# Optimization experiments

Hardware: AMD Instinct MI355X
Metric: run time of the kernel (lower is better)

## Reference

```python
import jax, jax.numpy as jnp
import numpy as np

# Dimensions (match init_kwargs)
B, N, D = 128, 256, 256   # batch, n_agents, obs_dim
MSG = 64                  # msg_dim
CD = 32                   # compressed_dim = int(msg_dim * 0.5)
K = 8                     # top-k recipients
H1, H2 = 128, 256         # msg_gen hidden, receiver hidden


def setup_inputs() -> dict:
    key = jax.random.key(0)
    ks = jax.random.split(key, 16)
    s = 0.02
    # All weights stored (in_features, out_features): y = x @ W + b
    return {
        "obs_all": jax.random.normal(ks[0], (B, N, D), dtype=jnp.float32),
        "W1": jax.random.normal(ks[1], (D, H1), dtype=jnp.float32) * s,
        "b1": jnp.zeros((H1,), jnp.float32),
        "W2": jax.random.normal(ks[2], (H1, MSG), dtype=jnp.float32) * s,
        "b2": jnp.zeros((MSG,), jnp.float32),
        "Wc": jax.random.normal(ks[3], (MSG, CD), dtype=jnp.float32) * s,
        "bc": jnp.zeros((CD,), jnp.float32),
        "Wd": jax.random.normal(ks[4], (CD, MSG), dtype=jnp.float32) * s,
        "bd": jnp.zeros((MSG,), jnp.float32),
        "Wbil": jax.random.normal(ks[5], (D, D), dtype=jnp.float32) * s,  # Bilinear weight (out=1)
        "bbil": jnp.zeros((), jnp.float32),
        "Wr1": jax.random.normal(ks[6], (D + MSG, H2), dtype=jnp.float32) * s,
        "br1": jnp.zeros((H2,), jnp.float32),
        "Wr2": jax.random.normal(ks[7], (H2, D), dtype=jnp.float32) * s,
        "br2": jnp.zeros((D,), jnp.float32),
    }


def reference(obs_all, W1, b1, W2, b2, Wc, bc, Wd, bd, Wbil, bbil, Wr1, br1, Wr2, br2):
    # send: msg_gen MLP -> compress -> decompress (all agents at once)
    h = jax.nn.relu(jnp.einsum('bnd,dh->bnh', obs_all, W1) + b1)
    full_msg = jnp.einsum('bnh,hm->bnm', h, W2) + b2          # (B, N, MSG)
    compressed = jnp.einsum('bnm,mc->bnc', full_msg, Wc) + bc  # (B, N, CD)
    msgs = jnp.einsum('bnc,cm->bnm', compressed, Wd) + bd      # (B, N, MSG)

    # pairwise bilinear relevance: scores[b,i,j] = obs_i^T Wbil obs_j + bias
    tmp = jnp.einsum('bid,de->bie', obs_all, Wbil)
    scores = jnp.einsum('bie,bje->bij', tmp, obs_all) + bbil   # (B, N, N)

    # top-k gating: softmax over the k selected scores, zeros elsewhere
    topk_vals, topk_idx = jax.lax.top_k(scores, K)             # (B, N, K)
    gate_vals = jax.nn.softmax(topk_vals, axis=-1)             # (B, N, K)

    # weighted aggregation of selected messages (honor top-k sparsity:
    # gather the K messages per receiver instead of building dense gates)
    sel_msgs = jax.vmap(lambda m, ix: m[ix])(msgs, topk_idx)   # (B, N, K, MSG)
    agg = jnp.einsum('bik,bikm->bim', gate_vals, sel_msgs)     # (B, N, MSG)

    # receive: MLP over [obs, aggregated message]
    combined = jnp.concatenate([obs_all, agg], axis=-1)        # (B, N, D+MSG)
    r = jax.nn.relu(jnp.einsum('bnc,ch->bnh', combined, Wr1) + br1)
    enriched = jnp.einsum('bnh,hd->bnd', r, Wr2) + br2          # (B, N, D)
    return enriched
```

## Files before the change

kernel.cpp:

```cpp
#include <hip/hip_runtime.h>
#include <cstddef>

#define BB   128
#define NN   256
#define DIMD 256
#define MSG  64
#define CDIM 32
#define TOPK 8
#define H1D  128
#define H2D  256
#define BN   (BB*NN)

typedef unsigned short u16;
typedef u16   u16x4  __attribute__((ext_vector_type(4)));
typedef u16   u16x8  __attribute__((ext_vector_type(8)));
typedef short short8 __attribute__((ext_vector_type(8)));
typedef float f32x4  __attribute__((ext_vector_type(4)));

__device__ __forceinline__ u16 f2bf(float f) {
    return (u16)((__float_as_uint(f) + 0x8000u) >> 16);
}
__device__ __forceinline__ float bf2f(u16 u) {
    return __uint_as_float(((unsigned)u) << 16);
}
__device__ __forceinline__ u16 bf2key(u16 b) {
    return (u16)(b ^ ((b & 0x8000u) ? 0xFFFFu : 0x8000u));
}
__device__ __forceinline__ u16 key2bf(u16 k) {
    return (u16)(k ^ ((k & 0x8000u) ? 0x8000u : 0xFFFFu));
}
#define MFMA16(a,b,c) __builtin_amdgcn_mfma_f32_16x16x32_bf16((a),(b),(c),0,0,0)


__global__ __launch_bounds__(256) void prep_w_k(
    const float* __restrict__ W1, const float* __restrict__ W2,
    const float* __restrict__ Wc, const float* __restrict__ Wd,
    const float* __restrict__ Wb, const float* __restrict__ Wr1,
    const float* __restrict__ Wr2,
    u16* __restrict__ Wp1, u16* __restrict__ Wp2, u16* __restrict__ Wpc,
    u16* __restrict__ Wpd, u16* __restrict__ WpB, u16* __restrict__ Wpr1,
    u16* __restrict__ Wpr2)
{
    const int t = blockIdx.x * 256 + threadIdx.x;
    const float* src; u16* dst; int I, os, loc;
    if      (t <  32768) { src = W1;  dst = Wp1;  I = 256; os = 7; loc = t; }
    else if (t <  40960) { src = W2;  dst = Wp2;  I = 128; os = 6; loc = t - 32768; }
    else if (t <  43008) { src = Wc;  dst = Wpc;  I = 64;  os = 5; loc = t - 40960; }
    else if (t <  45056) { src = Wd;  dst = Wpd;  I = 32;  os = 6; loc = t - 43008; }
    else if (t < 110592) { src = Wb;  dst = WpB;  I = 256; os = 8; loc = t - 45056; }
    else if (t < 192512) { src = Wr1; dst = Wpr1; I = 320; os = 8; loc = t - 110592; }
    else                 { src = Wr2; dst = Wpr2; I = 256; os = 8; loc = t - 192512; }
    const int i = loc >> os;
    const int o = loc & ((1 << os) - 1);
    const int nt = o >> 4, ls = o & 15;
    const int KB = I >> 5;
    const int kk = i >> 5, q = (i & 31) >> 3, j = i & 7;
    dst[((size_t)(nt*KB + kk)*64 + q*16 + ls)*8 + j] = f2bf(src[loc]);
}

__global__ __launch_bounds__(256) __attribute__((amdgpu_waves_per_eu(4, 4)))
void sendpack_k(
    const float* __restrict__ obs, u16* __restrict__ obs_p,
    const u16* __restrict__ Wp1, const float* __restrict__ b1,
    const u16* __restrict__ Wp2, const float* __restrict__ b2,
    const u16* __restrict__ Wpc, const float* __restrict__ bc,
    const u16* __restrict__ Wpd, const float* __restrict__ bd,
    u16* __restrict__ msgs_bf)
{
    __shared__ __align__(16) u16 sO[32][264];
    __shared__ __align__(16) u16 sH[32][136];
    __shared__ __align__(16) u16 sF[32][72];
    __shared__ __align__(16) u16 sC[32][40];
    const int t = threadIdx.x;
    const int w = t >> 6, l = t & 63, q = l >> 4, ls = l & 15;
    const int row0 = blockIdx.x * 32;
    const int tile0 = blockIdx.x * 2;

    {
        const float4* src = (const float4*)(obs + (size_t)row0 * 256);
        #pragma unroll
        for (int i = 0; i < 8; ++i) {
            const int idx = t + 256*i;
            const int r = idx >> 6, c4 = idx & 63;
            const float4 v = src[idx];
            u16x4 o;
            o[0] = f2bf(v.x); o[1] = f2bf(v.y); o[2] = f2bf(v.z); o[3] = f2bf(v.w);
            *(u16x4*)&sO[r][c4*4] = o;
        }
    }
    __syncthreads();
    {
        #pragma unroll
        for (int i = 0; i < 4; ++i) {
            const int u = t + 256*i;
            const int tile = u >> 9, kk = (u >> 6) & 7, lane = u & 63;
            const u16x8 v = *(const u16x8*)&sO[tile*16 + (lane & 15)][kk*32 + (lane >> 4)*8];
            *(u16x8*)(obs_p + (size_t)(tile0 + tile)*4096 + (size_t)(kk*64 + lane)*8) = v;
        }
    }
    {
        f32x4 acc[2][2];
        #pragma unroll
        for (int mi = 0; mi < 2; ++mi)
            #pragma unroll
            for (int nn = 0; nn < 2; ++nn) acc[mi][nn] = (f32x4){0,0,0,0};
        short8 cb[2];
        #pragma unroll
        for (int nn = 0; nn < 2; ++nn)
            cb[nn] = *(const short8*)(Wp1 + ((size_t)((w*2+nn)*8))*512 + l*8);
        #pragma unroll
        for (int kk = 0; kk < 8; ++kk) {
            short8 nb[2];
            if (kk < 7) {
                #pragma unroll
                for (int nn = 0; nn < 2; ++nn)
                    nb[nn] = *(const short8*)(Wp1 + ((size_t)((w*2+nn)*8 + kk+1))*512 + l*8);
            }
            short8 a[2];
            a[0] = *(const short8*)&sO[ls][kk*32 + q*8];
            a[1] = *(const short8*)&sO[16 + ls][kk*32 + q*8];
            #pragma unroll
            for (int mi = 0; mi < 2; ++mi)
                #pragma unroll
                for (int nn = 0; nn < 2; ++nn)
                    acc[mi][nn] = MFMA16(a[mi], cb[nn], acc[mi][nn]);
            if (kk < 7) {
                #pragma unroll
                for (int nn = 0; nn < 2; ++nn) cb[nn] = nb[nn];
            }
        }
        #pragma unroll
        for (int nn = 0; nn < 2; ++nn) {
            const float bv = b1[(w*2+nn)*16 + ls];
            #pragma unroll
            for (int mi = 0; mi < 2; ++mi)
                #pragma unroll
                for (int r = 0; r < 4; ++r)
                    sH[mi*16 + q*4 + r][(w*2+nn)*16 + ls] = f2bf(fmaxf(acc[mi][nn][r] + bv, 0.0f));
        }
    }
    __syncthreads();
    {
        f32x4 acc[2];
        acc[0] = (f32x4){0,0,0,0}; acc[1] = (f32x4){0,0,0,0};
        #pragma unroll
        for (int kk = 0; kk < 4; ++kk) {
            const int k0 = kk * 32;
            short8 a[2];
            a[0] = *(const short8*)(&sH[ls][k0 + q*8]);
            a[1] = *(const short8*)(&sH[16 + ls][k0 + q*8]);
            const short8 bf = *(const short8*)(Wp2 + ((size_t)(w*4 + kk)*64 + l)*8);
            acc[0] = MFMA16(a[0], bf, acc[0]);
            acc[1] = MFMA16(a[1], bf, acc[1]);
        }
        const float bv = b2[w*16 + ls];
        #pragma unroll
        for (int mi = 0; mi < 2; ++mi)
            #pragma unroll
            for (int r = 0; r < 4; ++r)
                sF[mi*16 + q*4 + r][w*16 + ls] = f2bf(acc[mi][r] + bv);
    }
    __syncthreads();
    if (w < 2) {
        f32x4 acc[2];
        acc[0] = (f32x4){0,0,0,0}; acc[1] = (f32x4){0,0,0,0};
        #pragma unroll
        for (int kk = 0; kk < 2; ++kk) {
            const int k0 = kk * 32;
            short8 a[2];
            a[0] = *(const short8*)(&sF[ls][k0 + q*8]);
            a[1] = *(const short8*)(&sF[16 + ls][k0 + q*8]);
            const short8 bf = *(const short8*)(Wpc + ((size_t)(w*2 + kk)*64 + l)*8);
            acc[0] = MFMA16(a[0], bf, acc[0]);
            acc[1] = MFMA16(a[1], bf, acc[1]);
        }
        const float bv = bc[w*16 + ls];
        #pragma unroll
        for (int mi = 0; mi < 2; ++mi)
            #pragma unroll
            for (int r = 0; r < 4; ++r)
                sC[mi*16 + q*4 + r][w*16 + ls] = f2bf(acc[mi][r] + bv);
    }
    __syncthreads();
    {
        f32x4 acc[2];
        acc[0] = (f32x4){0,0,0,0}; acc[1] = (f32x4){0,0,0,0};
        short8 a[2];
        a[0] = *(const short8*)(&sC[ls][q*8]);
        a[1] = *(const short8*)(&sC[16 + ls][q*8]);
        const short8 bf = *(const short8*)(Wpd + ((size_t)w*64 + l)*8);
        acc[0] = MFMA16(a[0], bf, acc[0]);
        acc[1] = MFMA16(a[1], bf, acc[1]);
        const float bv = bd[w*16 + ls];
        #pragma unroll
        for (int mi = 0; mi < 2; ++mi)
            #pragma unroll
            for (int r = 0; r < 4; ++r)
                msgs_bf[(size_t)(row0 + mi*16 + q*4 + r)*MSG + w*16 + ls] = f2bf(acc[mi][r] + bv);
    }
}

__global__ __launch_bounds__(512) __attribute__((amdgpu_waves_per_eu(4, 4)))
void relrecv_k(
    const u16* __restrict__ obs_p, const u16* __restrict__ WpB,
    const float* __restrict__ bbil, const u16* __restrict__ msgs_bf,
    const u16* __restrict__ Wpr1, const float* __restrict__ br1,
    const u16* __restrict__ Wpr2, const float* __restrict__ br2,
    float* __restrict__ out)
{
    __shared__ __align__(16) u16 sS[64][264];
    __shared__ __align__(16) u16 sA[64][72];
    __shared__ __align__(16) u16 sObs[16384];
    __shared__ float sG[64][8];
    __shared__ unsigned short sI[64][8];
    const int t = threadIdx.x;
    const int w = t >> 6, l = t & 63, q = l >> 4, ls = l & 15;
    const int bid = blockIdx.x;
    const int xcd = bid & 7, idx = bid >> 3;
    const int b   = xcd * 16 + (idx >> 2);
    const int mc  = idx & 3;
    const int row0g = b * NN + mc * 64;
    const int mt0   = b * 16 + mc * 4;

    short8 pb[4][2];

    {
        const u16x8* src = (const u16x8*)(obs_p + (size_t)mt0 * 4096);
        #pragma unroll
        for (int i = 0; i < 4; ++i)
            *(u16x8*)&sObs[(t + 512*i) * 8] = src[t + 512*i];
    }
    #pragma unroll
    for (int d = 0; d < 3; ++d)
        #pragma unroll
        for (int nn = 0; nn < 2; ++nn)
            pb[d][nn] = *(const short8*)(WpB + ((size_t)((w*2+nn)*8 + d))*512 + l*8);
    __syncthreads();

    {
        f32x4 acc[4][2];
        #pragma unroll
        for (int mi = 0; mi < 4; ++mi)
            #pragma unroll
            for (int nn = 0; nn < 2; ++nn) acc[mi][nn] = (f32x4){0,0,0,0};
        #pragma unroll
        for (int kk = 0; kk < 8; ++kk) {
            if (kk < 5) {
                #pragma unroll
                for (int nn = 0; nn < 2; ++nn)
                    pb[(kk+3)&3][nn] = *(const short8*)(WpB + ((size_t)((w*2+nn)*8 + kk+3))*512 + l*8);
            }
            short8 a[4];
            #pragma unroll
            for (int mi = 0; mi < 4; ++mi)
                a[mi] = *(const short8*)&sObs[mi*4096 + kk*512 + l*8];
            #pragma unroll
            for (int mi = 0; mi < 4; ++mi)
                #pragma unroll
                for (int nn = 0; nn < 2; ++nn)
                    acc[mi][nn] = MFMA16(a[mi], pb[kk&3][nn], acc[mi][nn]);
        }
        #pragma unroll
        for (int mi = 0; mi < 4; ++mi)
            #pragma unroll
            for (int nn = 0; nn < 2; ++nn)
                #pragma unroll
                for (int r = 0; r < 4; ++r)
                    sS[mi*16 + q*4 + r][(w*2+nn)*16 + ls] = f2bf(acc[mi][nn][r]);
    }
    #pragma unroll
    for (int d = 0; d < 3; ++d)
        #pragma unroll
        for (int nn = 0; nn < 2; ++nn)
            pb[d][nn] = *(const short8*)(obs_p + ((size_t)((b*16 + w*2+nn)*8 + d))*512 + l*8);
    __syncthreads();

    {
        const float bb = bbil[0];
        f32x4 acc[4][2];
        #pragma unroll
        for (int mi = 0; mi < 4; ++mi)
            #pragma unroll
            for (int nn = 0; nn < 2; ++nn) acc[mi][nn] = (f32x4){0,0,0,0};
        #pragma unroll
        for (int kk = 0; kk < 8; ++kk) {
            if (kk < 5) {
                #pragma unroll
                for (int nn = 0; nn < 2; ++nn)
                    pb[(kk+3)&3][nn] = *(const short8*)(obs_p + ((size_t)((b*16 + w*2+nn)*8 + kk+3))*512 + l*8);
            }
            const int k0 = kk * 32;
            short8 a[4];
            #pragma unroll
            for (int mi = 0; mi < 4; ++mi)
                a[mi] = *(const short8*)(&sS[mi*16 + ls][k0 + q*8]);
            #pragma unroll
            for (int mi = 0; mi < 4; ++mi)
                #pragma unroll
                for (int nn = 0; nn < 2; ++nn)
                    acc[mi][nn] = MFMA16(a[mi], pb[kk&3][nn], acc[mi][nn]);
        }
        __syncthreads();
        #pragma unroll
        for (int mi = 0; mi < 4; ++mi)
            #pragma unroll
            for (int nn = 0; nn < 2; ++nn)
                #pragma unroll
                for (int r = 0; r < 4; ++r)
                    sS[mi*16 + q*4 + r][(w*2+nn)*16 + ls] = bf2key(f2bf(acc[mi][nn][r] + bb));
    }
    __syncthreads();
    {
        const int r = t >> 3, g = t & 7;
        u16 buf[32];
        #pragma unroll
        for (int c = 0; c < 4; ++c)
            *(u16x8*)&buf[c*8] = *(const u16x8*)&sS[r][g*32 + c*8];
        unsigned val[8];
        #pragma unroll
        for (int j = 0; j < 8; ++j) val[j] = 0u;
        #pragma unroll
        for (int i = 0; i < 32; ++i) {
            const unsigned p = ((unsigned)buf[i] << 8) | (unsigned)(255 - (g*32 + i));
            if (p > val[7]) {
                #pragma unroll
                for (int j = 7; j >= 1; --j) {
                    const bool cj  = p > val[j];
                    const bool cjm = p > val[j-1];
                    val[j] = cj ? (cjm ? val[j-1] : p) : val[j];
                }
                val[0] = p > val[0] ? p : val[0];
            }
        }
        unsigned wv[8];
        #pragma unroll
        for (int k = 0; k < 8; ++k) {
            unsigned h = val[0], o;
            o = (unsigned)__shfl_xor((int)h, 1); h = o > h ? o : h;
            o = (unsigned)__shfl_xor((int)h, 2); h = o > h ? o : h;
            o = (unsigned)__shfl_xor((int)h, 4); h = o > h ? o : h;
            wv[k] = h;
            const bool won = (val[0] == h);
            #pragma unroll
            for (int j = 0; j < 7; ++j) val[j] = won ? val[j+1] : val[j];
            val[7] = won ? 0u : val[7];
        }
        if (g == 0) {
            float v[8];
            #pragma unroll
            for (int k = 0; k < 8; ++k)
                v[k] = bf2f(key2bf((u16)(wv[k] >> 8)));
            float e[8]; float s = 0.0f;
            #pragma unroll
            for (int k = 0; k < 8; ++k) { e[k] = __expf(v[k] - v[0]); s += e[k]; }
            const float inv = 1.0f / s;
            #pragma unroll
            for (int k = 0; k < 8; ++k) {
                sG[r][k] = e[k] * inv;
                sI[r][k] = (unsigned short)(255 - (wv[k] & 255u));
            }
        }
    }
    #pragma unroll
    for (int d = 0; d < 3; ++d)
        #pragma unroll
        for (int nn = 0; nn < 2; ++nn)
            pb[d][nn] = *(const short8*)(Wpr1 + ((size_t)((w*2+nn)*10 + d))*512 + l*8);
    {
        const u16* mb = msgs_bf + (size_t)b*NN*MSG + l;
        #pragma unroll
        for (int rr = 0; rr < 8; ++rr) {
            const int row = w*8 + rr;
            u16 mv[8];
            #pragma unroll
            for (int k = 0; k < 8; ++k)
                mv[k] = mb[(size_t)sI[row][k]*MSG];
            float a = 0.0f;
            #pragma unroll
            for (int k = 0; k < 8; ++k)
                a = fmaf(sG[row][k], bf2f(mv[k]), a);
            sA[row][l] = f2bf(a);
        }
    }
    __syncthreads();
    {
        f32x4 acc[4][2];
        #pragma unroll
        for (int mi = 0; mi < 4; ++mi)
            #pragma unroll
            for (int nn = 0; nn < 2; ++nn) acc[mi][nn] = (f32x4){0,0,0,0};
        #pragma unroll
        for (int kk = 0; kk < 10; ++kk) {
            if (kk < 7) {
                #pragma unroll
                for (int nn = 0; nn < 2; ++nn)
                    pb[(kk+3)&3][nn] = *(const short8*)(Wpr1 + ((size_t)((w*2+nn)*10 + kk+3))*512 + l*8);
            }
            short8 a[4];
            if (kk < 8) {
                #pragma unroll
                for (int mi = 0; mi < 4; ++mi)
                    a[mi] = *(const short8*)&sObs[mi*4096 + kk*512 + l*8];
            } else {
                #pragma unroll
                for (int mi = 0; mi < 4; ++mi)
                    a[mi] = *(const short8*)&sA[mi*16 + ls][(kk-8)*32 + q*8];
            }
            #pragma unroll
            for (int mi = 0; mi < 4; ++mi)
                #pragma unroll
                for (int nn = 0; nn < 2; ++nn)
                    acc[mi][nn] = MFMA16(a[mi], pb[kk&3][nn], acc[mi][nn]);
        }
        #pragma unroll
        for (int d = 0; d < 3; ++d)
            #pragma unroll
            for (int nn = 0; nn < 2; ++nn)
                pb[d][nn] = *(const short8*)(Wpr2 + ((size_t)((w*2+nn)*8 + d))*512 + l*8);
        __syncthreads();
        #pragma unroll
        for (int nn = 0; nn < 2; ++nn) {
            const float bv = br1[(w*2+nn)*16 + ls];
            #pragma unroll
            for (int mi = 0; mi < 4; ++mi)
                #pragma unroll
                for (int r = 0; r < 4; ++r)
                    sS[mi*16 + q*4 + r][(w*2+nn)*16 + ls] = f2bf(fmaxf(acc[mi][nn][r] + bv, 0.0f));
        }
    }
    __syncthreads();
    {
        f32x4 acc[4][2];
        #pragma unroll
        for (int mi = 0; mi < 4; ++mi)
            #pragma unroll
            for (int nn = 0; nn < 2; ++nn) acc[mi][nn] = (f32x4){0,0,0,0};
        #pragma unroll
        for (int kk = 0; kk < 8; ++kk) {
            if (kk < 5) {
                #pragma unroll
                for (int nn = 0; nn < 2; ++nn)
                    pb[(kk+3)&3][nn] = *(const short8*)(Wpr2 + ((size_t)((w*2+nn)*8 + kk+3))*512 + l*8);
            }
            const int k0 = kk * 32;
            short8 a[4];
            #pragma unroll
            for (int mi = 0; mi < 4; ++mi)
                a[mi] = *(const short8*)(&sS[mi*16 + ls][k0 + q*8]);
            #pragma unroll
            for (int mi = 0; mi < 4; ++mi)
                #pragma unroll
                for (int nn = 0; nn < 2; ++nn)
                    acc[mi][nn] = MFMA16(a[mi], pb[kk&3][nn], acc[mi][nn]);
        }
        #pragma unroll
        for (int nn = 0; nn < 2; ++nn) {
            const float bv = br2[(w*2+nn)*16 + ls];
            #pragma unroll
            for (int mi = 0; mi < 4; ++mi)
                #pragma unroll
                for (int r = 0; r < 4; ++r)
                    out[(size_t)(row0g + mi*16 + q*4 + r)*DIMD + (w*2+nn)*16 + ls] = acc[mi][nn][r] + bv;
        }
    }
}

extern "C" void kernel_launch(void* const* d_in, const int* in_sizes, int n_in,
                              void* d_out, int out_size, void* d_ws, size_t ws_size,
                              hipStream_t stream)
{
    (void)in_sizes; (void)n_in; (void)out_size; (void)ws_size;
    const float* obs  = (const float*)d_in[0];
    const float* W1   = (const float*)d_in[1];
    const float* b1   = (const float*)d_in[2];
    const float* W2   = (const float*)d_in[3];
    const float* b2   = (const float*)d_in[4];
    const float* Wc   = (const float*)d_in[5];
    const float* bc   = (const float*)d_in[6];
    const float* Wd   = (const float*)d_in[7];
    const float* bd   = (const float*)d_in[8];
    const float* Wbil = (const float*)d_in[9];
    const float* bbil = (const float*)d_in[10];
    const float* Wr1  = (const float*)d_in[11];
    const float* br1  = (const float*)d_in[12];
    const float* Wr2  = (const float*)d_in[13];
    const float* br2  = (const float*)d_in[14];
    float* outp = (float*)d_out;

    u16* obs_p   = (u16*)d_ws;
    u16* msgs_bf = obs_p   + (size_t)BN*256;
    u16* Wp1  = msgs_bf + (size_t)BN*64;
    u16* Wp2  = Wp1  + 32768;
    u16* Wpc  = Wp2  + 8192;
    u16* Wpd  = Wpc  + 2048;
    u16* WpB  = Wpd  + 2048;
    u16* Wpr1 = WpB  + 65536;
    u16* Wpr2 = Wpr1 + 81920;

    prep_w_k<<<1008, 256, 0, stream>>>(W1, W2, Wc, Wd, Wbil, Wr1, Wr2,
                                       Wp1, Wp2, Wpc, Wpd, WpB, Wpr1, Wpr2);
    sendpack_k<<<BN/32, 256, 0, stream>>>(obs, obs_p, Wp1, b1, Wp2, b2,
                                          Wpc, bc, Wpd, bd, msgs_bf);
    relrecv_k<<<BN/64, 512, 0, stream>>>(obs_p, WpB, bbil, msgs_bf,
                                         Wpr1, br1, Wpr2, br2, outp);
}
```

Before: 56.37 us.

## Double relrecv block to 1024 threads with one N-tile per wave

The fused relevance/top-k/receive kernel now runs 16 waves per block instead of 8. Each wave computes a single 16-column output tile per GEMM stage instead of two. The top-k scan splits each row across 16 lanes of 16 scores and adds one more shuffle-reduction step. The goal is more latency hiding and less per-wave register pressure for the same LDS footprint, at the cost of larger blocks and barrier synchronization across more waves.

```diff
diff --git a/kernel.cpp b/kernel.cpp
--- a/kernel.cpp
+++ b/kernel.cpp
@@ -200,7 +200,7 @@
     }
 }
 
-__global__ __launch_bounds__(512) __attribute__((amdgpu_waves_per_eu(4, 4)))
+__global__ __launch_bounds__(1024) __attribute__((amdgpu_waves_per_eu(8, 8)))
 void relrecv_k(
     const u16* __restrict__ obs_p, const u16* __restrict__ WpB,
     const float* __restrict__ bbil, const u16* __restrict__ msgs_bf,
@@ -222,73 +222,55 @@
     const int row0g = b * NN + mc * 64;
     const int mt0   = b * 16 + mc * 4;
 
-    short8 pb[4][2];
+    short8 pb[4];
 
     {
         const u16x8* src = (const u16x8*)(obs_p + (size_t)mt0 * 4096);
         #pragma unroll
-        for (int i = 0; i < 4; ++i)
-            *(u16x8*)&sObs[(t + 512*i) * 8] = src[t + 512*i];
+        for (int i = 0; i < 2; ++i)
+            *(u16x8*)&sObs[(t + 1024*i) * 8] = src[t + 1024*i];
     }
     #pragma unroll
     for (int d = 0; d < 3; ++d)
-        #pragma unroll
-        for (int nn = 0; nn < 2; ++nn)
-            pb[d][nn] = *(const short8*)(WpB + ((size_t)((w*2+nn)*8 + d))*512 + l*8);
-    __syncthreads();
-
-    {
-        f32x4 acc[4][2];
+        pb[d] = *(const short8*)(WpB + ((size_t)(w*8 + d))*512 + l*8);
+    __syncthreads();
+
+    {
+        f32x4 acc[4];
+        #pragma unroll
+        for (int mi = 0; mi < 4; ++mi) acc[mi] = (f32x4){0,0,0,0};
+        #pragma unroll
+        for (int kk = 0; kk < 8; ++kk) {
+            if (kk < 5)
+                pb[(kk+3)&3] = *(const short8*)(WpB + ((size_t)(w*8 + kk+3))*512 + l*8);
+            short8 a[4];
+            #pragma unroll
+            for (int mi = 0; mi < 4; ++mi)
+                a[mi] = *(const short8*)&sObs[mi*4096 + kk*512 + l*8];
+            #pragma unroll
+            for (int mi = 0; mi < 4; ++mi)
+                acc[mi] = MFMA16(a[mi], pb[kk&3], acc[mi]);
+        }
         #pragma unroll
         for (int mi = 0; mi < 4; ++mi)
             #pragma unroll
-            for (int nn = 0; nn < 2; ++nn) acc[mi][nn] = (f32x4){0,0,0,0};
-        #pragma unroll
-        for (int kk = 0; kk < 8; ++kk) {
-            if (kk < 5) {
-                #pragma unroll
-                for (int nn = 0; nn < 2; ++nn)
-                    pb[(kk+3)&3][nn] = *(const short8*)(WpB + ((size_t)((w*2+nn)*8 + kk+3))*512 + l*8);
-            }
-            short8 a[4];
-            #pragma unroll
-            for (int mi = 0; mi < 4; ++mi)
-                a[mi] = *(const short8*)&sObs[mi*4096 + kk*512 + l*8];
-            #pragma unroll
-            for (int mi = 0; mi < 4; ++mi)
-                #pragma unroll
-                for (int nn = 0; nn < 2; ++nn)
-                    acc[mi][nn] = MFMA16(a[mi], pb[kk&3][nn], acc[mi][nn]);
-        }
-        #pragma unroll
-        for (int mi = 0; mi < 4; ++mi)
-            #pragma unroll
-            for (int nn = 0; nn < 2; ++nn)
-                #pragma unroll
-                for (int r = 0; r < 4; ++r)
-                    sS[mi*16 + q*4 + r][(w*2+nn)*16 + ls] = f2bf(acc[mi][nn][r]);
+            for (int r = 0; r < 4; ++r)
+                sS[mi*16 + q*4 + r][w*16 + ls] = f2bf(acc[mi][r]);
     }
     #pragma unroll
     for (int d = 0; d < 3; ++d)
-        #pragma unroll
-        for (int nn = 0; nn < 2; ++nn)
-            pb[d][nn] = *(const short8*)(obs_p + ((size_t)((b*16 + w*2+nn)*8 + d))*512 + l*8);
+        pb[d] = *(const short8*)(obs_p + ((size_t)((b*16 + w)*8 + d))*512 + l*8);
     __syncthreads();
 
     {
         const float bb = bbil[0];
-        f32x4 acc[4][2];
-        #pragma unroll
-        for (int mi = 0; mi < 4; ++mi)
-            #pragma unroll
-            for (int nn = 0; nn < 2; ++nn) acc[mi][nn] = (f32x4){0,0,0,0};
+        f32x4 acc[4];
+        #pragma unroll
+        for (int mi = 0; mi < 4; ++mi) acc[mi] = (f32x4){0,0,0,0};
         #pragma unroll
         for (int kk = 0; kk < 8; ++kk) {
-            if (kk < 5) {
-                #pragma unroll
-                for (int nn = 0; nn < 2; ++nn)
-                    pb[(kk+3)&3][nn] = *(const short8*)(obs_p + ((size_t)((b*16 + w*2+nn)*8 + kk+3))*512 + l*8);
-            }
+            if (kk < 5)
+                pb[(kk+3)&3] = *(const short8*)(obs_p + ((size_t)((b*16 + w)*8 + kk+3))*512 + l*8);
             const int k0 = kk * 32;
             short8 a[4];
             #pragma unroll
@@ -296,32 +278,28 @@
                 a[mi] = *(const short8*)(&sS[mi*16 + ls][k0 + q*8]);
             #pragma unroll
             for (int mi = 0; mi < 4; ++mi)
-                #pragma unroll
-                for (int nn = 0; nn < 2; ++nn)
-                    acc[mi][nn] = MFMA16(a[mi], pb[kk&3][nn], acc[mi][nn]);
+                acc[mi] = MFMA16(a[mi], pb[kk&3], acc[mi]);
         }
         __syncthreads();
         #pragma unroll
         for (int mi = 0; mi < 4; ++mi)
             #pragma unroll
-            for (int nn = 0; nn < 2; ++nn)
-                #pragma unroll
-                for (int r = 0; r < 4; ++r)
-                    sS[mi*16 + q*4 + r][(w*2+nn)*16 + ls] = bf2key(f2bf(acc[mi][nn][r] + bb));
-    }
-    __syncthreads();
-    {
-        const int r = t >> 3, g = t & 7;
-        u16 buf[32];
-        #pragma unroll
-        for (int c = 0; c < 4; ++c)
-            *(u16x8*)&buf[c*8] = *(const u16x8*)&sS[r][g*32 + c*8];
+            for (int r = 0; r < 4; ++r)
+                sS[mi*16 + q*4 + r][w*16 + ls] = bf2key(f2bf(acc[mi][r] + bb));
+    }
+    __syncthreads();
+    {
+        const int r = t >> 4, g = t & 15;
+        u16 buf[16];
+        #pragma unroll
+        for (int c = 0; c < 2; ++c)
+            *(u16x8*)&buf[c*8] = *(const u16x8*)&sS[r][g*16 + c*8];
         unsigned val[8];
         #pragma unroll
         for (int j = 0; j < 8; ++j) val[j] = 0u;
         #pragma unroll
-        for (int i = 0; i < 32; ++i) {
-            const unsigned p = ((unsigned)buf[i] << 8) | (unsigned)(255 - (g*32 + i));
+        for (int i = 0; i < 16; ++i) {
+            const unsigned p = ((unsigned)buf[i] << 8) | (unsigned)(255 - (g*16 + i));
             if (p > val[7]) {
                 #pragma unroll
                 for (int j = 7; j >= 1; --j) {
@@ -339,6 +317,7 @@
             o = (unsigned)__shfl_xor((int)h, 1); h = o > h ? o : h;
             o = (unsigned)__shfl_xor((int)h, 2); h = o > h ? o : h;
             o = (unsigned)__shfl_xor((int)h, 4); h = o > h ? o : h;
+            o = (unsigned)__shfl_xor((int)h, 8); h = o > h ? o : h;
             wv[k] = h;
             const bool won = (val[0] == h);
             #pragma unroll
@@ -363,14 +342,12 @@
     }
     #pragma unroll
     for (int d = 0; d < 3; ++d)
-        #pragma unroll
-        for (int nn = 0; nn < 2; ++nn)
-            pb[d][nn] = *(const short8*)(Wpr1 + ((size_t)((w*2+nn)*10 + d))*512 + l*8);
+        pb[d] = *(const short8*)(Wpr1 + ((size_t)(w*10 + d))*512 + l*8);
     {
         const u16* mb = msgs_bf + (size_t)b*NN*MSG + l;
         #pragma unroll
-        for (int rr = 0; rr < 8; ++rr) {
-            const int row = w*8 + rr;
+        for (int rr = 0; rr < 4; ++rr) {
+            const int row = w*4 + rr;
             u16 mv[8];
             #pragma unroll
             for (int k = 0; k < 8; ++k)
@@ -384,18 +361,13 @@
     }
     __syncthreads();
     {
-        f32x4 acc[4][2];
-        #pragma unroll
-        for (int mi = 0; mi < 4; ++mi)
-            #pragma unroll
-            for (int nn = 0; nn < 2; ++nn) acc[mi][nn] = (f32x4){0,0,0,0};
+        f32x4 acc[4];
+        #pragma unroll
+        for (int mi = 0; mi < 4; ++mi) acc[mi] = (f32x4){0,0,0,0};
         #pragma unroll
         for (int kk = 0; kk < 10; ++kk) {
-            if (kk < 7) {
-                #pragma unroll
-                for (int nn = 0; nn < 2; ++nn)
-                    pb[(kk+3)&3][nn] = *(const short8*)(Wpr1 + ((size_t)((w*2+nn)*10 + kk+3))*512 + l*8);
-            }
+            if (kk < 7)
+                pb[(kk+3)&3] = *(const short8*)(Wpr1 + ((size_t)(w*10 + kk+3))*512 + l*8);
             short8 a[4];
             if (kk < 8) {
                 #pragma unroll
@@ -408,40 +380,28 @@
             }
             #pragma unroll
             for (int mi = 0; mi < 4; ++mi)
-                #pragma unroll
-                for (int nn = 0; nn < 2; ++nn)
-                    acc[mi][nn] = MFMA16(a[mi], pb[kk&3][nn], acc[mi][nn]);
+                acc[mi] = MFMA16(a[mi], pb[kk&3], acc[mi]);
         }
         #pragma unroll
         for (int d = 0; d < 3; ++d)
-            #pragma unroll
-            for (int nn = 0; nn < 2; ++nn)
-                pb[d][nn] = *(const short8*)(Wpr2 + ((size_t)((w*2+nn)*8 + d))*512 + l*8);
+            pb[d] = *(const short8*)(Wpr2 + ((size_t)(w*8 + d))*512 + l*8);
         __syncthreads();
-        #pragma unroll
-        for (int nn = 0; nn < 2; ++nn) {
-            const float bv = br1[(w*2+nn)*16 + ls];
-            #pragma unroll
-            for (int mi = 0; mi < 4; ++mi)
-                #pragma unroll
-                for (int r = 0; r < 4; ++r)
-                    sS[mi*16 + q*4 + r][(w*2+nn)*16 + ls] = f2bf(fmaxf(acc[mi][nn][r] + bv, 0.0f));
-        }
-    }
-    __syncthreads();
-    {
-        f32x4 acc[4][2];
+        const float bv = br1[w*16 + ls];
         #pragma unroll
         for (int mi = 0; mi < 4; ++mi)
             #pragma unroll
-            for (int nn = 0; nn < 2; ++nn) acc[mi][nn] = (f32x4){0,0,0,0};
+            for (int r = 0; r < 4; ++r)
+                sS[mi*16 + q*4 + r][w*16 + ls] = f2bf(fmaxf(acc[mi][r] + bv, 0.0f));
+    }
+    __syncthreads();
+    {
+        f32x4 acc[4];
+        #pragma unroll
+        for (int mi = 0; mi < 4; ++mi) acc[mi] = (f32x4){0,0,0,0};
         #pragma unroll
         for (int kk = 0; kk < 8; ++kk) {
-            if (kk < 5) {
-                #pragma unroll
-                for (int nn = 0; nn < 2; ++nn)
-                    pb[(kk+3)&3][nn] = *(const short8*)(Wpr2 + ((size_t)((w*2+nn)*8 + kk+3))*512 + l*8);
-            }
+            if (kk < 5)
+                pb[(kk+3)&3] = *(const short8*)(Wpr2 + ((size_t)(w*8 + kk+3))*512 + l*8);
             const int k0 = kk * 32;
             short8 a[4];
             #pragma unroll
@@ -449,19 +409,14 @@
                 a[mi] = *(const short8*)(&sS[mi*16 + ls][k0 + q*8]);
             #pragma unroll
             for (int mi = 0; mi < 4; ++mi)
-                #pragma unroll
-                for (int nn = 0; nn < 2; ++nn)
-                    acc[mi][nn] = MFMA16(a[mi], pb[kk&3][nn], acc[mi][nn]);
-        }
-        #pragma unroll
-        for (int nn = 0; nn < 2; ++nn) {
-            const float bv = br2[(w*2+nn)*16 + ls];
-            #pragma unroll
-            for (int mi = 0; mi < 4; ++mi)
-                #pragma unroll
-                for (int r = 0; r < 4; ++r)
-                    out[(size_t)(row0g + mi*16 + q*4 + r)*DIMD + (w*2+nn)*16 + ls] = acc[mi][nn][r] + bv;
-        }
+                acc[mi] = MFMA16(a[mi], pb[kk&3], acc[mi]);
+        }
+        const float bv = br2[w*16 + ls];
+        #pragma unroll
+        for (int mi = 0; mi < 4; ++mi)
+            #pragma unroll
+            for (int r = 0; r < 4; ++r)
+                out[(size_t)(row0g + mi*16 + q*4 + r)*DIMD + w*16 + ls] = acc[mi][r] + bv;
     }
 }
 
@@ -501,6 +456,6 @@
                                        Wp1, Wp2, Wpc, Wpd, WpB, Wpr1, Wpr2);
     sendpack_k<<<BN/32, 256, 0, stream>>>(obs, obs_p, Wp1, b1, Wp2, b2,
                                           Wpc, bc, Wpd, bd, msgs_bf);
-    relrecv_k<<<BN/64, 512, 0, stream>>>(obs_p, WpB, bbil, msgs_bf,
-                                         Wpr1, br1, Wpr2, br2, outp);
-}
+    relrecv_k<<<BN/64, 1024, 0, stream>>>(obs_p, WpB, bbil, msgs_bf,
+                                          Wpr1, br1, Wpr2, br2, outp);
+}
```

Measured after the change: 59.53 us. +5.6%, slower.

## Fuse receiver layer-1 obs partial product into bilinear first GEMM loop

Applied to the files above, without the earlier changes.

The obs-part of the receiver's first layer (obs @ Wr1[:256]) is now accumulated in the same k-loop as obs @ Wbil, reusing the A fragments loaded from shared memory, into a persistent accumulator. After aggregation only the two message k-slices are added. Weight prefetch changes from a 3-deep ring to double buffering. This removes a second pass over sObs and shortens the post-topk critical path. The cost is 32 more live accumulator registers across the whole kernel, which may reduce occupancy or cause spills.

```diff
diff --git a/kernel.cpp b/kernel.cpp
--- a/kernel.cpp
+++ b/kernel.cpp
@@ -222,7 +222,13 @@
     const int row0g = b * NN + mc * 64;
     const int mt0   = b * 16 + mc * 4;
 
-    short8 pb[4][2];
+    short8 pbB[2][2];
+    short8 pbW[2][2];
+    f32x4  accL1[4][2];
+    #pragma unroll
+    for (int mi = 0; mi < 4; ++mi)
+        #pragma unroll
+        for (int nn = 0; nn < 2; ++nn) accL1[mi][nn] = (f32x4){0,0,0,0};
 
     {
         const u16x8* src = (const u16x8*)(obs_p + (size_t)mt0 * 4096);
@@ -231,10 +237,10 @@
             *(u16x8*)&sObs[(t + 512*i) * 8] = src[t + 512*i];
     }
     #pragma unroll
-    for (int d = 0; d < 3; ++d)
-        #pragma unroll
-        for (int nn = 0; nn < 2; ++nn)
-            pb[d][nn] = *(const short8*)(WpB + ((size_t)((w*2+nn)*8 + d))*512 + l*8);
+    for (int nn = 0; nn < 2; ++nn) {
+        pbB[0][nn] = *(const short8*)(WpB  + ((size_t)((w*2+nn)*8))*512  + l*8);
+        pbW[0][nn] = *(const short8*)(Wpr1 + ((size_t)((w*2+nn)*10))*512 + l*8);
+    }
     __syncthreads();
 
     {
@@ -245,10 +251,13 @@
             for (int nn = 0; nn < 2; ++nn) acc[mi][nn] = (f32x4){0,0,0,0};
         #pragma unroll
         for (int kk = 0; kk < 8; ++kk) {
-            if (kk < 5) {
-                #pragma unroll
-                for (int nn = 0; nn < 2; ++nn)
-                    pb[(kk+3)&3][nn] = *(const short8*)(WpB + ((size_t)((w*2+nn)*8 + kk+3))*512 + l*8);
+            const int cur = kk & 1, nxt = cur ^ 1;
+            if (kk < 7) {
+                #pragma unroll
+                for (int nn = 0; nn < 2; ++nn) {
+                    pbB[nxt][nn] = *(const short8*)(WpB  + ((size_t)((w*2+nn)*8  + kk+1))*512 + l*8);
+                    pbW[nxt][nn] = *(const short8*)(Wpr1 + ((size_t)((w*2+nn)*10 + kk+1))*512 + l*8);
+                }
             }
             short8 a[4];
             #pragma unroll
@@ -257,8 +266,10 @@
             #pragma unroll
             for (int mi = 0; mi < 4; ++mi)
                 #pragma unroll
-                for (int nn = 0; nn < 2; ++nn)
-                    acc[mi][nn] = MFMA16(a[mi], pb[kk&3][nn], acc[mi][nn]);
+                for (int nn = 0; nn < 2; ++nn) {
+                    acc[mi][nn]   = MFMA16(a[mi], pbB[cur][nn], acc[mi][nn]);
+                    accL1[mi][nn] = MFMA16(a[mi], pbW[cur][nn], accL1[mi][nn]);
+                }
         }
         #pragma unroll
         for (int mi = 0; mi < 4; ++mi)
@@ -269,10 +280,8 @@
                     sS[mi*16 + q*4 + r][(w*2+nn)*16 + ls] = f2bf(acc[mi][nn][r]);
     }
     #pragma unroll
-    for (int d = 0; d < 3; ++d)
-        #pragma unroll
-        for (int nn = 0; nn < 2; ++nn)
-            pb[d][nn] = *(const short8*)(obs_p + ((size_t)((b*16 + w*2+nn)*8 + d))*512 + l*8);
+    for (int nn = 0; nn < 2; ++nn)
+        pbB[0][nn] = *(const short8*)(obs_p + ((size_t)((b*16 + w*2+nn)*8))*512 + l*8);
     __syncthreads();
 
     {
@@ -284,10 +293,11 @@
             for (int nn = 0; nn < 2; ++nn) acc[mi][nn] = (f32x4){0,0,0,0};
         #pragma unroll
         for (int kk = 0; kk < 8; ++kk) {
-            if (kk < 5) {
-                #pragma unroll
-                for (int nn = 0; nn < 2; ++nn)
-                    pb[(kk+3)&3][nn] = *(const short8*)(obs_p + ((size_t)((b*16 + w*2+nn)*8 + kk+3))*512 + l*8);
+            const int cur = kk & 1, nxt = cur ^ 1;
+            if (kk < 7) {
+                #pragma unroll
+                for (int nn = 0; nn < 2; ++nn)
+                    pbB[nxt][nn] = *(const short8*)(obs_p + ((size_t)((b*16 + w*2+nn)*8 + kk+1))*512 + l*8);
             }
             const int k0 = kk * 32;
             short8 a[4];
@@ -298,7 +308,7 @@
             for (int mi = 0; mi < 4; ++mi)
                 #pragma unroll
                 for (int nn = 0; nn < 2; ++nn)
-                    acc[mi][nn] = MFMA16(a[mi], pb[kk&3][nn], acc[mi][nn]);
+                    acc[mi][nn] = MFMA16(a[mi], pbB[cur][nn], acc[mi][nn]);
         }
         __syncthreads();
         #pragma unroll
@@ -361,11 +371,12 @@
             }
         }
     }
+    short8 pwA[2][2];
     #pragma unroll
-    for (int d = 0; d < 3; ++d)
+    for (int d = 0; d < 2; ++d)
         #pragma unroll
         for (int nn = 0; nn < 2; ++nn)
-            pb[d][nn] = *(const short8*)(Wpr1 + ((size_t)((w*2+nn)*10 + d))*512 + l*8);
+            pwA[d][nn] = *(const short8*)(Wpr1 + ((size_t)((w*2+nn)*10 + 8 + d))*512 + l*8);
     {
         const u16* mb = msgs_bf + (size_t)b*NN*MSG + l;
         #pragma unroll
@@ -384,40 +395,21 @@
     }
     __syncthreads();
     {
-        f32x4 acc[4][2];
-        #pragma unroll
-        for (int mi = 0; mi < 4; ++mi)
-            #pragma unroll
-            for (int nn = 0; nn < 2; ++nn) acc[mi][nn] = (f32x4){0,0,0,0};
-        #pragma unroll
-        for (int kk = 0; kk < 10; ++kk) {
-            if (kk < 7) {
-                #pragma unroll
-                for (int nn = 0; nn < 2; ++nn)
-                    pb[(kk+3)&3][nn] = *(const short8*)(Wpr1 + ((size_t)((w*2+nn)*10 + kk+3))*512 + l*8);
-            }
+        #pragma unroll
+        for (int d = 0; d < 2; ++d) {
             short8 a[4];
-            if (kk < 8) {
-                #pragma unroll
-                for (int mi = 0; mi < 4; ++mi)
-                    a[mi] = *(const short8*)&sObs[mi*4096 + kk*512 + l*8];
-            } else {
-                #pragma unroll
-                for (int mi = 0; mi < 4; ++mi)
-                    a[mi] = *(const short8*)&sA[mi*16 + ls][(kk-8)*32 + q*8];
-            }
-            #pragma unroll
-            for (int mi = 0; mi < 4; ++mi)
-                #pragma unroll
-                for (int nn = 0; nn < 2; ++nn)
-                    acc[mi][nn] = MFMA16(a[mi], pb[kk&3][nn], acc[mi][nn]);
-        }
-        #pragma unroll
-        for (int d = 0; d < 3; ++d)
-            #pragma unroll
-            for (int nn = 0; nn < 2; ++nn)
-                pb[d][nn] = *(const short8*)(Wpr2 + ((size_t)((w*2+nn)*8 + d))*512 + l*8);
-        __syncthreads();
+            #pragma unroll
+            for (int mi = 0; mi < 4; ++mi)
+                a[mi] = *(const short8*)&sA[mi*16 + ls][d*32 + q*8];
+            #pragma unroll
+            for (int mi = 0; mi < 4; ++mi)
+                #pragma unroll
+                for (int nn = 0; nn < 2; ++nn)
+                    accL1[mi][nn] = MFMA16(a[mi], pwA[d][nn], accL1[mi][nn]);
+        }
+        #pragma unroll
+        for (int nn = 0; nn < 2; ++nn)
+            pbB[0][nn] = *(const short8*)(Wpr2 + ((size_t)((w*2+nn)*8))*512 + l*8);
         #pragma unroll
         for (int nn = 0; nn < 2; ++nn) {
             const float bv = br1[(w*2+nn)*16 + ls];
@@ -425,7 +417,7 @@
             for (int mi = 0; mi < 4; ++mi)
                 #pragma unroll
                 for (int r = 0; r < 4; ++r)
-                    sS[mi*16 + q*4 + r][(w*2+nn)*16 + ls] = f2bf(fmaxf(acc[mi][nn][r] + bv, 0.0f));
+                    sS[mi*16 + q*4 + r][(w*2+nn)*16 + ls] = f2bf(fmaxf(accL1[mi][nn][r] + bv, 0.0f));
         }
     }
     __syncthreads();
@@ -437,10 +429,11 @@
             for (int nn = 0; nn < 2; ++nn) acc[mi][nn] = (f32x4){0,0,0,0};
         #pragma unroll
         for (int kk = 0; kk < 8; ++kk) {
-            if (kk < 5) {
-                #pragma unroll
-                for (int nn = 0; nn < 2; ++nn)
-                    pb[(kk+3)&3][nn] = *(const short8*)(Wpr2 + ((size_t)((w*2+nn)*8 + kk+3))*512 + l*8);
+            const int cur = kk & 1, nxt = cur ^ 1;
+            if (kk < 7) {
+                #pragma unroll
+                for (int nn = 0; nn < 2; ++nn)
+                    pbB[nxt][nn] = *(const short8*)(Wpr2 + ((size_t)((w*2+nn)*8 + kk+1))*512 + l*8);
             }
             const int k0 = kk * 32;
             short8 a[4];
@@ -451,7 +444,7 @@
             for (int mi = 0; mi < 4; ++mi)
                 #pragma unroll
                 for (int nn = 0; nn < 2; ++nn)
-                    acc[mi][nn] = MFMA16(a[mi], pb[kk&3][nn], acc[mi][nn]);
+                    acc[mi][nn] = MFMA16(a[mi], pbB[cur][nn], acc[mi][nn]);
         }
         #pragma unroll
         for (int nn = 0; nn < 2; ++nn) {
```

New measurement: 60.63 us. +7.6%, slower.
